# Kernel optimization log

Measured on AMD Instinct MI355X. Metric: run time of the kernel, lower is better.

Reference implementation:

```python
import jax, jax.numpy as jnp
import numpy as np

B, L, C, H, W = 1, 16, 16, 128, 256  # L = T_chunk = K_chunk (single chunk, causal)
DECAY = 0.1  # decay_val


def setup_inputs() -> dict:
    key = jax.random.key(0)
    k1, k2 = jax.random.split(key)
    img = jax.random.normal(k1, (B, L, C, H, W), jnp.float32)
    # flows in normalized [-1,1] grid units; keep displacements modest
    cum_flow = jax.random.normal(k2, (B, L, 2, H, W), jnp.float32) * 0.1
    t = jnp.arange(L)
    mask = (t[:, None] >= t[None, :]).astype(jnp.float32)          # causal [T,K]
    decay_dist = jnp.abs(t[:, None] - t[None, :]).astype(jnp.float32)  # [T,K]
    return {"img": img, "cum_flow": cum_flow, "mask": mask, "decay_dist": decay_dist}


def _bilinear_sample(img, gx, gy):
    # img: [B,K,C,H,W]; gx, gy: [B,K,H,W] in normalized [-1,1] coords.
    # x wraps around (periodic), y clamps -- matching the kernel's index handling.
    ix = (gx + 1.0) * (W * 0.5) - 0.5
    iy = (gy + 1.0) * (H * 0.5) - 0.5
    x0 = jnp.floor(ix)
    y0 = jnp.floor(iy)
    wx = ix - x0  # fractional weights
    wy = iy - y0
    x0i = x0.astype(jnp.int32)
    y0i = y0.astype(jnp.int32)
    x0r = jnp.mod(x0i, W)
    x1r = jnpp = jnp.mod(x0i + 1, W)
    y0c = jnp.clip(y0i, 0, H - 1)
    y1c = jnp.clip(y0i + 1, 0, H - 1)

    K = img.shape[1]
    imgf = img.reshape(B, K, C, H * W)

    def gather(yy, xx):
        idx = (yy * W + xx).reshape(B, K, 1, H * W)  # broadcast over C
        return jnp.take_along_axis(imgf, idx, axis=-1).reshape(B, K, C, H, W)

    va = gather(y0c, x0r)  # (y0, x0)
    vb = gather(y1c, x0r)  # (y1, x0)
    vc = gather(y0c, x1r)  # (y0, x1)
    vd = gather(y1c, x1r)  # (y1, x1)
    wx_ = wx[:, :, None]   # [B,K,1,H,W]
    wy_ = wy[:, :, None]
    return (va * (1.0 - wx_) * (1.0 - wy_) + vb * (1.0 - wx_) * wy_
            + vc * wx_ * (1.0 - wy_) + vd * wx_ * wy_)


def reference(img, cum_flow, mask, decay_dist):
    # base grid (align_corners=False style pixel centers)
    base_x = (jnp.arange(W, dtype=jnp.float32) * (2.0 / W) - 1.0 + 1.0 / W)[None, None, :]  # [1,1,W]
    base_y = (jnp.arange(H, dtype=jnp.float32) * (2.0 / H) - 1.0 + 1.0 / H)[None, :, None]  # [1,H,1]

    weights = mask * jnp.exp(-DECAY * decay_dist)  # [T,K] decay-weighted causal mask
    fx = cum_flow[:, :, 0]  # [B,L,H,W]
    fy = cum_flow[:, :, 1]

    def step(carry, inp):
        ft_x, ft_y, w_row = inp  # ft_*: [B,H,W]; w_row: [K]
        gx = base_x[None] + (ft_x[:, None] - fx)  # [B,K,H,W]
        gy = base_y[None] + (ft_y[:, None] - fy)
        gx = jnp.mod(gx + 1.0, 2.0) - 1.0          # wrap x into [-1,1)
        sampled = _bilinear_sample(img, gx, gy)    # [B,K,C,H,W]
        out_t = jnp.einsum('k,bkchw->bchw', w_row, sampled)
        return carry, out_t

    xs = (jnp.moveaxis(fx, 1, 0), jnp.moveaxis(fy, 1, 0), weights)  # over t
    _, outs = jax.lax.scan(step, 0.0, xs)          # [T,B,C,H,W]
    return jnp.moveaxis(outs, 0, 1)                # [B,T,C,H,W]
```

## Files before the change

### kernel.cpp

```cpp
#include <hip/hip_runtime.h>

constexpr int Lc = 16;
constexpr int Cc = 16;
constexpr int Hc = 128;
constexpr int Wc = 256;
constexpr float DECAYc = 0.1f;
constexpr int HWc = Hc * Wc;

__device__ inline unsigned short f2bf(float f) {
    unsigned int u = __float_as_uint(f);
    u += 0x7fffu + ((u >> 16) & 1u);
    return (unsigned short)(u >> 16);
}
__device__ inline float2 bf2f2(unsigned int u) {
    return make_float2(__uint_as_float(u << 16),
                       __uint_as_float(u & 0xffff0000u));
}

__global__ __launch_bounds__(256) void transpose_cvt_bf16(
    const float* __restrict__ img, unsigned short* __restrict__ imgTb)
{
    const int tid = threadIdx.x;
    const int h2 = tid & 1;
    const int wq = tid >> 1;
    const int kf  = blockIdx.x >> 5;
    const int px0 = (blockIdx.x & 31) * 1024;
    const float* __restrict__ srcb = img + (size_t)kf * Cc * HWc + (size_t)(8 * h2) * HWc;
#pragma unroll
    for (int rr = 0; rr < 8; ++rr) {
        const int px = px0 + rr * 128 + wq;
        float v[8];
#pragma unroll
        for (int c = 0; c < 8; ++c) v[c] = srcb[c * HWc + px];
        uint4 o;
        o.x = (unsigned int)f2bf(v[0]) | ((unsigned int)f2bf(v[1]) << 16);
        o.y = (unsigned int)f2bf(v[2]) | ((unsigned int)f2bf(v[3]) << 16);
        o.z = (unsigned int)f2bf(v[4]) | ((unsigned int)f2bf(v[5]) << 16);
        o.w = (unsigned int)f2bf(v[6]) | ((unsigned int)f2bf(v[7]) << 16);
        *(uint4*)(imgTb + ((size_t)kf * HWc + px) * Cc + 8 * h2) = o;
    }
}

template <int T0>
__device__ inline void do_chunk(
    int k, const unsigned short* __restrict__ bk, int q, int pix,
    const float* sx1, const float* sy1, float fxk, float fyk,
    const float* __restrict__ wtab, float4* acc)
{
    int   offs[4][4];
    float wts [4][4];
    uint2 ld  [4][4];

#pragma unroll
    for (int j = 0; j < 4; ++j) {
        const int t = T0 + j;
        if (t >= Lc) continue;
        if (t > k) {
            const float wkt = wtab[t * Lc + k];
            float m = sx1[t] - fxk;
            m -= 2.0f * floorf(m * 0.5f);
            const float ix = m * (Wc * 0.5f) - 0.5f;
            const float iy = (sy1[t] - fyk) * (Hc * 0.5f) - 0.5f;
            const float x0f = floorf(ix);
            const float y0f = floorf(iy);
            const float wx = ix - x0f;
            const float wy = iy - y0f;
            const int x0 = (int)x0f;
            const int y0 = (int)y0f;
            const int x0r = x0 & (Wc - 1);
            const int x1r = (x0 + 1) & (Wc - 1);
            const int y0c = min(max(y0, 0), Hc - 1);
            const int y1c = min(max(y0 + 1, 0), Hc - 1);
            const float wb = wkt * wy;
            const float wa = wkt - wb;
            const float omx = 1.0f - wx;
            wts[j][0] = wa * omx;
            wts[j][1] = wa * wx;
            wts[j][2] = wb * omx;
            wts[j][3] = wb * wx;
            offs[j][0] = y0c * Wc + x0r;
            offs[j][1] = y0c * Wc + x1r;
            offs[j][2] = y1c * Wc + x0r;
            offs[j][3] = y1c * Wc + x1r;
        }
    }
#pragma unroll
    for (int j = 0; j < 4; ++j) {
        const int t = T0 + j;
        if (t >= Lc) continue;
        if (t > k) {
#pragma unroll
            for (int n = 0; n < 4; ++n)
                ld[j][n] = ((const uint2*)(bk + (size_t)offs[j][n] * Cc))[q];
        }
    }
#pragma unroll
    for (int j = 0; j < 4; ++j) {
        const int t = T0 + j;
        if (t >= Lc) continue;
        if (t > k) {
#pragma unroll
            for (int n = 0; n < 4; ++n) {
                const float2 f01 = bf2f2(ld[j][n].x);
                const float2 f23 = bf2f2(ld[j][n].y);
                const float a = wts[j][n];
                acc[t].x += a * f01.x;
                acc[t].y += a * f01.y;
                acc[t].z += a * f23.x;
                acc[t].w += a * f23.y;
            }
        }
    }
}

__global__ __launch_bounds__(256) void gridsample_bf16(
    const unsigned short* __restrict__ imgTb,
    const float* __restrict__ cum_flow,
    const float* __restrict__ mask,
    const float* __restrict__ decay,
    const float* __restrict__ img,
    float* __restrict__ out)
{
    __shared__ float wtab[Lc * Lc];
    const int tid = threadIdx.x;
    if (tid < Lc * Lc)
        wtab[tid] = mask[tid] * __expf(-DECAYc * decay[tid]);
    __syncthreads();

    const int q  = tid & 3;
    const int wq = tid >> 2;
    const int b = blockIdx.x;
    const int band = b & 7;
    const int sub  = b >> 3;
    const int h = band * 16 + (sub >> 2);
    const int w = (sub & 3) * 64 + wq;
    const int pix = h * Wc + w;

    const float base_x = w * (2.0f / Wc) - 1.0f + 1.0f / Wc;
    const float base_y = h * (2.0f / Hc) - 1.0f + 1.0f / Hc;

    float sx1[Lc], sy1[Lc];
#pragma unroll
    for (int t = 0; t < Lc; ++t) {
        sx1[t] = base_x + cum_flow[(t * 2 + 0) * HWc + pix] + 1.0f;
        sy1[t] = base_y + cum_flow[(t * 2 + 1) * HWc + pix] + 1.0f;
    }

    float4 acc[Lc];
#pragma unroll
    for (int t = 0; t < Lc; ++t) acc[t] = make_float4(0.f, 0.f, 0.f, 0.f);

    for (int k = 0; k < Lc - 1; ++k) {
        const float fxk = cum_flow[(k * 2 + 0) * HWc + pix];
        const float fyk = cum_flow[(k * 2 + 1) * HWc + pix];
        const unsigned short* __restrict__ bk = imgTb + (size_t)k * HWc * Cc;

        do_chunk<1> (k, bk, q, pix, sx1, sy1, fxk, fyk, wtab, acc);
        do_chunk<5> (k, bk, q, pix, sx1, sy1, fxk, fyk, wtab, acc);
        do_chunk<9> (k, bk, q, pix, sx1, sy1, fxk, fyk, wtab, acc);
        do_chunk<13>(k, bk, q, pix, sx1, sy1, fxk, fyk, wtab, acc);
    }

#pragma unroll
    for (int t = 0; t < Lc; ++t) {
        const float* __restrict__ ip = img + ((size_t)t * Cc + 4 * q) * HWc + pix;
        float* __restrict__ op = out + ((size_t)t * Cc + 4 * q) * HWc + pix;
        op[0 * HWc] = acc[t].x + ip[0 * HWc];
        op[1 * HWc] = acc[t].y + ip[1 * HWc];
        op[2 * HWc] = acc[t].z + ip[2 * HWc];
        op[3 * HWc] = acc[t].w + ip[3 * HWc];
    }
}

__global__ __launch_bounds__(256) void gridsample_warp_acc(
    const float* __restrict__ img, const float* __restrict__ cum_flow,
    const float* __restrict__ mask, const float* __restrict__ decay,
    float* __restrict__ out)
{
    const int w = threadIdx.x, h = blockIdx.x, t = blockIdx.y;
    const int pix = h * Wc + w;
    const float base_x = w * (2.0f / Wc) - 1.0f + 1.0f / Wc;
    const float base_y = h * (2.0f / Hc) - 1.0f + 1.0f / Hc;
    const float fxt = cum_flow[(t * 2 + 0) * HWc + pix];
    const float fyt = cum_flow[(t * 2 + 1) * HWc + pix];
    float acc[Cc];
#pragma unroll
    for (int c = 0; c < Cc; ++c) acc[c] = 0.0f;
    for (int k = 0; k <= t; ++k) {
        const float wkt = mask[t * Lc + k] * __expf(-DECAYc * decay[t * Lc + k]);
        const float fxk = cum_flow[(k * 2 + 0) * HWc + pix];
        const float fyk = cum_flow[(k * 2 + 1) * HWc + pix];
        float gx = base_x + (fxt - fxk);
        const float gy = base_y + (fyt - fyk);
        float m = gx + 1.0f;
        m -= 2.0f * floorf(m * 0.5f);
        gx = m - 1.0f;
        const float ix = (gx + 1.0f) * (Wc * 0.5f) - 0.5f;
        const float iy = (gy + 1.0f) * (Hc * 0.5f) - 0.5f;
        const float x0f = floorf(ix), y0f = floorf(iy);
        const float wx = ix - x0f, wy = iy - y0f;
        const int x0 = (int)x0f, y0 = (int)y0f;
        const int x0r = x0 & (Wc - 1), x1r = (x0 + 1) & (Wc - 1);
        const int y0c = min(max(y0, 0), Hc - 1), y1c = min(max(y0 + 1, 0), Hc - 1);
        const float a00 = wkt * (1.0f - wx) * (1.0f - wy);
        const float a01 = wkt * (1.0f - wx) * wy;
        const float a10 = wkt * wx * (1.0f - wy);
        const float a11 = wkt * wx * wy;
        const int o00 = y0c * Wc + x0r, o01 = y1c * Wc + x0r;
        const int o10 = y0c * Wc + x1r, o11 = y1c * Wc + x1r;
        const float* __restrict__ ik = img + (size_t)k * Cc * HWc;
#pragma unroll
        for (int c = 0; c < Cc; ++c) {
            const float* __restrict__ p = ik + c * HWc;
            acc[c] += p[o00] * a00 + p[o01] * a01 + p[o10] * a10 + p[o11] * a11;
        }
    }
    float* __restrict__ op = out + (size_t)t * Cc * HWc + pix;
#pragma unroll
    for (int c = 0; c < Cc; ++c) op[c * HWc] = acc[c];
}

extern "C" void kernel_launch(void* const* d_in, const int* in_sizes, int n_in,
                              void* d_out, int out_size, void* d_ws, size_t ws_size,
                              hipStream_t stream) {
    const float* img      = (const float*)d_in[0];
    const float* cum_flow = (const float*)d_in[1];
    const float* mask     = (const float*)d_in[2];
    const float* decay    = (const float*)d_in[3];
    float* out = (float*)d_out;

    const size_t needed = (size_t)Lc * HWc * Cc * sizeof(unsigned short);
    if (ws_size >= needed) {
        unsigned short* imgTb = (unsigned short*)d_ws;
        transpose_cvt_bf16<<<dim3(512), 256, 0, stream>>>(img, imgTb);
        gridsample_bf16<<<dim3(512), 256, 0, stream>>>(
            imgTb, cum_flow, mask, decay, img, out);
    } else {
        dim3 grid(Hc, Lc, 1);
        gridsample_warp_acc<<<grid, Wc, 0, stream>>>(img, cum_flow, mask, decay, out);
    }
}
```

Measured before the change: 151.0 us.

## Split timesteps into four load-balanced groups across blocks to raise parallelism

Partitions the 16 output timesteps into four masks of equal causal work and launches four times as many blocks, each handling one timestep subset. Each thread then holds far fewer accumulators and sampling coordinates, cutting register pressure, and a minimum-occupancy hint is added to the launch bounds. The cost is redundant per-k flow loads and block setup repeated across the four groups.

```diff
diff --git a/kernel.cpp b/kernel.cpp
--- a/kernel.cpp
+++ b/kernel.cpp
@@ -16,6 +16,8 @@
     return make_float2(__uint_as_float(u << 16),
                        __uint_as_float(u & 0xffff0000u));
 }
+
+constexpr int topbit(unsigned m) { int r = 0; while (m >>= 1) ++r; return r; }
 
 __global__ __launch_bounds__(256) void transpose_cvt_bf16(
     const float* __restrict__ img, unsigned short* __restrict__ imgTb)
@@ -41,21 +43,22 @@
     }
 }
 
-template <int T0>
-__device__ inline void do_chunk(
-    int k, const unsigned short* __restrict__ bk, int q, int pix,
+template <unsigned MASK, int TLO, int THI>
+__device__ __forceinline__ void do_chunk_m(
+    int k, const unsigned short* __restrict__ bk, int q,
     const float* sx1, const float* sy1, float fxk, float fyk,
     const float* __restrict__ wtab, float4* acc)
 {
-    int   offs[4][4];
-    float wts [4][4];
-    uint2 ld  [4][4];
-
-#pragma unroll
-    for (int j = 0; j < 4; ++j) {
-        const int t = T0 + j;
-        if (t >= Lc) continue;
+    constexpr int NT = THI - TLO + 1;
+    int   offs[NT][4];
+    float wts [NT][4];
+    uint2 ld  [NT][4];
+
+#pragma unroll
+    for (int t = TLO; t <= THI; ++t) {
+        if (!((MASK >> t) & 1u)) continue;
         if (t > k) {
+            const int j = t - TLO;
             const float wkt = wtab[t * Lc + k];
             float m = sx1[t] - fxk;
             m -= 2.0f * floorf(m * 0.5f);
@@ -85,20 +88,20 @@
         }
     }
 #pragma unroll
-    for (int j = 0; j < 4; ++j) {
-        const int t = T0 + j;
-        if (t >= Lc) continue;
+    for (int t = TLO; t <= THI; ++t) {
+        if (!((MASK >> t) & 1u)) continue;
         if (t > k) {
+            const int j = t - TLO;
 #pragma unroll
             for (int n = 0; n < 4; ++n)
                 ld[j][n] = ((const uint2*)(bk + (size_t)offs[j][n] * Cc))[q];
         }
     }
 #pragma unroll
-    for (int j = 0; j < 4; ++j) {
-        const int t = T0 + j;
-        if (t >= Lc) continue;
+    for (int t = TLO; t <= THI; ++t) {
+        if (!((MASK >> t) & 1u)) continue;
         if (t > k) {
+            const int j = t - TLO;
 #pragma unroll
             for (int n = 0; n < 4; ++n) {
                 const float2 f01 = bf2f2(ld[j][n].x);
@@ -113,7 +116,50 @@
     }
 }
 
-__global__ __launch_bounds__(256) void gridsample_bf16(
+template <unsigned MASK>
+__device__ __forceinline__ void run_quarter(
+    const unsigned short* __restrict__ imgTb,
+    const float* __restrict__ cum_flow,
+    const float* __restrict__ img,
+    float* __restrict__ out,
+    const float* wtab,
+    int q, int pix, float base_x, float base_y)
+{
+    float sx1[Lc], sy1[Lc];
+#pragma unroll
+    for (int t = 0; t < Lc; ++t) {
+        if (!((MASK >> t) & 1u)) continue;
+        sx1[t] = base_x + cum_flow[(t * 2 + 0) * HWc + pix] + 1.0f;
+        sy1[t] = base_y + cum_flow[(t * 2 + 1) * HWc + pix] + 1.0f;
+    }
+
+    float4 acc[Lc];
+#pragma unroll
+    for (int t = 0; t < Lc; ++t)
+        if ((MASK >> t) & 1u) acc[t] = make_float4(0.f, 0.f, 0.f, 0.f);
+
+    constexpr int KMAX = topbit(MASK);
+    for (int k = 0; k < KMAX; ++k) {
+        const float fxk = cum_flow[(k * 2 + 0) * HWc + pix];
+        const float fyk = cum_flow[(k * 2 + 1) * HWc + pix];
+        const unsigned short* __restrict__ bk = imgTb + (size_t)k * HWc * Cc;
+        do_chunk_m<MASK, 1, 7>(k, bk, q, sx1, sy1, fxk, fyk, wtab, acc);
+        do_chunk_m<MASK, 8, 15>(k, bk, q, sx1, sy1, fxk, fyk, wtab, acc);
+    }
+
+#pragma unroll
+    for (int t = 0; t < Lc; ++t) {
+        if (!((MASK >> t) & 1u)) continue;
+        const float* __restrict__ ip = img + ((size_t)t * Cc + 4 * q) * HWc + pix;
+        float* __restrict__ op = out + ((size_t)t * Cc + 4 * q) * HWc + pix;
+        op[0 * HWc] = acc[t].x + ip[0 * HWc];
+        op[1 * HWc] = acc[t].y + ip[1 * HWc];
+        op[2 * HWc] = acc[t].z + ip[2 * HWc];
+        op[3 * HWc] = acc[t].w + ip[3 * HWc];
+    }
+}
+
+__global__ __launch_bounds__(256, 6) void gridsample_bf16_tq(
     const unsigned short* __restrict__ imgTb,
     const float* __restrict__ cum_flow,
     const float* __restrict__ mask,
@@ -129,9 +175,11 @@
 
     const int q  = tid & 3;
     const int wq = tid >> 2;
-    const int b = blockIdx.x;
-    const int band = b & 7;
-    const int sub  = b >> 3;
+    const int b  = blockIdx.x;
+    const int quarter = b >> 9;
+    const int pb = b & 511;
+    const int band = pb & 7;
+    const int sub  = pb >> 3;
     const int h = band * 16 + (sub >> 2);
     const int w = (sub & 3) * 64 + wq;
     const int pix = h * Wc + w;
@@ -139,36 +187,11 @@
     const float base_x = w * (2.0f / Wc) - 1.0f + 1.0f / Wc;
     const float base_y = h * (2.0f / Hc) - 1.0f + 1.0f / Hc;
 
-    float sx1[Lc], sy1[Lc];
-#pragma unroll
-    for (int t = 0; t < Lc; ++t) {
-        sx1[t] = base_x + cum_flow[(t * 2 + 0) * HWc + pix] + 1.0f;
-        sy1[t] = base_y + cum_flow[(t * 2 + 1) * HWc + pix] + 1.0f;
-    }
-
-    float4 acc[Lc];
-#pragma unroll
-    for (int t = 0; t < Lc; ++t) acc[t] = make_float4(0.f, 0.f, 0.f, 0.f);
-
-    for (int k = 0; k < Lc - 1; ++k) {
-        const float fxk = cum_flow[(k * 2 + 0) * HWc + pix];
-        const float fyk = cum_flow[(k * 2 + 1) * HWc + pix];
-        const unsigned short* __restrict__ bk = imgTb + (size_t)k * HWc * Cc;
-
-        do_chunk<1> (k, bk, q, pix, sx1, sy1, fxk, fyk, wtab, acc);
-        do_chunk<5> (k, bk, q, pix, sx1, sy1, fxk, fyk, wtab, acc);
-        do_chunk<9> (k, bk, q, pix, sx1, sy1, fxk, fyk, wtab, acc);
-        do_chunk<13>(k, bk, q, pix, sx1, sy1, fxk, fyk, wtab, acc);
-    }
-
-#pragma unroll
-    for (int t = 0; t < Lc; ++t) {
-        const float* __restrict__ ip = img + ((size_t)t * Cc + 4 * q) * HWc + pix;
-        float* __restrict__ op = out + ((size_t)t * Cc + 4 * q) * HWc + pix;
-        op[0 * HWc] = acc[t].x + ip[0 * HWc];
-        op[1 * HWc] = acc[t].y + ip[1 * HWc];
-        op[2 * HWc] = acc[t].z + ip[2 * HWc];
-        op[3 * HWc] = acc[t].w + ip[3 * HWc];
+    switch (quarter) {
+        case 0:  run_quarter<0x8240u>(imgTb, cum_flow, img, out, wtab, q, pix, base_x, base_y); break;
+        case 1:  run_quarter<0x5010u>(imgTb, cum_flow, img, out, wtab, q, pix, base_x, base_y); break;
+        case 2:  run_quarter<0x280Eu>(imgTb, cum_flow, img, out, wtab, q, pix, base_x, base_y); break;
+        default: run_quarter<0x05A1u>(imgTb, cum_flow, img, out, wtab, q, pix, base_x, base_y); break;
     }
 }
 
@@ -233,7 +256,7 @@
     if (ws_size >= needed) {
         unsigned short* imgTb = (unsigned short*)d_ws;
         transpose_cvt_bf16<<<dim3(512), 256, 0, stream>>>(img, imgTb);
-        gridsample_bf16<<<dim3(512), 256, 0, stream>>>(
+        gridsample_bf16_tq<<<dim3(2048), 256, 0, stream>>>(
             imgTb, cum_flow, mask, decay, img, out);
     } else {
         dim3 grid(Hc, Lc, 1);
```

After: 164.6 us. +9.0%, slower.
